# Performance work log

Hardware: AMD Instinct MI355X
Metric: run time of the kernel (lower is better)

Reference implementation:

```python
import jax, jax.numpy as jnp
import numpy as np

N, E = 50000, 800000
D_IN_N, D_IN_E, D_OUT = 64, 64, 64


def setup_inputs() -> dict:
    key = jax.random.key(0)
    ks = jax.random.split(key, 10)
    stdv = 1.0 / np.sqrt(D_OUT)
    u = lambda k, shape: jax.random.uniform(k, shape, jnp.float32, -stdv, stdv)
    return {
        "nf": jax.random.normal(ks[0], (N, D_IN_N), jnp.float32),
        "ef": jax.random.normal(ks[1], (E, D_IN_E), jnp.float32),
        "src": jax.random.randint(ks[2], (E,), 0, N, jnp.int32),
        "dst": jax.random.randint(ks[3], (E,), 0, N, jnp.int32),
        "W_node": u(ks[4], (D_IN_N, D_OUT)),
        "W_edge": u(ks[5], (D_IN_E, D_OUT)),
        "bias_node": u(ks[6], (D_OUT,)),
        "bias_edge": u(ks[7], (D_OUT,)),
        "W_dense": u(ks[8], (2 * D_OUT, D_OUT)),  # Linear(2*out, out) weight, stored transposed
        "b_dense": u(ks[9], (D_OUT,)),
    }


def reference(nf, ef, src, dst, W_node, W_edge, bias_node, bias_edge, W_dense, b_dense):
    n_nodes = nf.shape[0]
    # input projections
    nf_h = nf @ W_node                     # [N, D]
    ef_h = ef @ W_edge                     # [E, D]
    # update_all: mean of incoming edge features per dst node (0 for isolated nodes, DGL default)
    deg = jax.ops.segment_sum(jnp.ones((ef_h.shape[0],), ef_h.dtype), dst, num_segments=n_nodes)
    nb_ef = jax.ops.segment_sum(ef_h, dst, num_segments=n_nodes) / jnp.maximum(deg, 1.0)[:, None]
    # apply_nodes: nf = act(nf + bias)
    nf_out = jax.nn.relu(nf_h + bias_node)
    # apply_edges (uses updated nf): cat([ef + nb_ef[dst], (nf[src]+nf[dst])/2]) -> Linear -> +bias -> act
    tmp_ef = ef_h + nb_ef[dst]             # [E, D]
    srcdst_nf = (nf_out[src] + nf_out[dst]) * 0.5
    ef_out = jnp.concatenate([tmp_ef, srcdst_nf], axis=1) @ W_dense + b_dense + bias_edge
    ef_out = jax.nn.relu(ef_out)
    return nf_out, ef_out
```

## Files before the change

kernel.cpp:

```cpp
#include <hip/hip_runtime.h>

#define D 64

typedef __attribute__((ext_vector_type(8))) short short8;
typedef __attribute__((ext_vector_type(4))) float f32x4;

__device__ __forceinline__ ushort f2b(float f) {
    union { float f; unsigned u; } x; x.f = f;
    unsigned r = x.u + 0x7FFFu + ((x.u >> 16) & 1u);
    return (ushort)(r >> 16);
}
__device__ __forceinline__ float b2f(ushort u) {
    union { float f; unsigned u; } x; x.u = ((unsigned)u) << 16;
    return x.f;
}
__device__ __forceinline__ short8 pack8(float4 a, float4 b) {
    short8 r;
    r[0] = (short)f2b(a.x); r[1] = (short)f2b(a.y); r[2] = (short)f2b(a.z); r[3] = (short)f2b(a.w);
    r[4] = (short)f2b(b.x); r[5] = (short)f2b(b.y); r[6] = (short)f2b(b.z); r[7] = (short)f2b(b.w);
    return r;
}

__global__ __launch_bounds__(256) void setup_kernel(
    const float* __restrict__ W_edge, const float* __restrict__ W_dense,
    const float* __restrict__ b_dense, const float* __restrict__ bias_edge,
    ushort* __restrict__ Wcomb_b, float* __restrict__ bias2)
{
    const int tid = threadIdx.x;
    for (int idx = tid; idx < D * D; idx += 256) {
        int k = idx >> 6, n = idx & 63;
        float s = 0.f;
        #pragma unroll 8
        for (int j = 0; j < D; ++j)
            s = fmaf(W_edge[k * D + j], W_dense[j * D + n], s);
        Wcomb_b[n * D + k] = f2b(s);
    }
    if (tid < D) bias2[tid] = b_dense[tid] + bias_edge[tid];
}

__global__ __launch_bounds__(256) void node_proj_kernel(
    const float* __restrict__ nf, const float* __restrict__ Wn,
    const float* __restrict__ bias, const float* __restrict__ Wd_bot,
    float* __restrict__ out, ushort* __restrict__ nfp_b, int N)
{
    constexpr int ROWS = 16;
    __shared__ float Ws[D * D];
    __shared__ float Wb[D * D];
    __shared__ float As[ROWS * D];
    __shared__ float Vs[ROWS * D];
    const int tid = threadIdx.x;
    const long row0 = (long)blockIdx.x * ROWS;

    #pragma unroll
    for (int i = tid; i < D * D / 4; i += 256) {
        ((float4*)Ws)[i] = ((const float4*)Wn)[i];
        float4 v = ((const float4*)Wd_bot)[i];
        ((float4*)Wb)[i] = make_float4(0.5f * v.x, 0.5f * v.y, 0.5f * v.z, 0.5f * v.w);
    }
    {
        int i = tid;
        long r = row0 + (i * 4) / D;
        ((float4*)As)[i] = (r < N) ? ((const float4*)nf)[row0 * D / 4 + i]
                                   : make_float4(0.f, 0.f, 0.f, 0.f);
    }
    __syncthreads();

    const int c = tid & 63;
    const float b = bias[c];
    for (int rr = tid >> 6; rr < ROWS; rr += 4) {
        float acc = 0.f;
        #pragma unroll
        for (int k = 0; k < D; ++k)
            acc = fmaf(As[rr * D + k], Ws[k * D + c], acc);
        float v = fmaxf(acc + b, 0.f);
        Vs[rr * D + c] = v;
        long r = row0 + rr;
        if (r < N) out[r * D + c] = v;
    }
    __syncthreads();
    for (int rr = tid >> 6; rr < ROWS; rr += 4) {
        float acc = 0.f;
        #pragma unroll
        for (int k = 0; k < D; ++k)
            acc = fmaf(Vs[rr * D + k], Wb[k * D + c], acc);
        long r = row0 + rr;
        if (r < N) nfp_b[r * D + c] = f2b(acc);
    }
}

__global__ __launch_bounds__(256) void hist_kernel(
    const int* __restrict__ dst, int* __restrict__ deg_i, int E)
{
    int i = blockIdx.x * 256 + threadIdx.x;
    if (i < E) atomicAdd(deg_i + dst[i], 1);
}

__global__ __launch_bounds__(256) void scanA_kernel(
    const int* __restrict__ deg_i, int* __restrict__ pos,
    int* __restrict__ bsum, int N)
{
    __shared__ int s[256];
    const int tid = threadIdx.x;
    const int i = blockIdx.x * 256 + tid;
    int v = (i < N) ? deg_i[i] : 0;
    s[tid] = v;
    __syncthreads();
    #pragma unroll
    for (int off = 1; off < 256; off <<= 1) {
        int t = (tid >= off) ? s[tid - off] : 0;
        __syncthreads();
        s[tid] += t;
        __syncthreads();
    }
    if (i < N) pos[i] = s[tid] - v;
    if (tid == 255) bsum[blockIdx.x] = s[255];
}

__global__ __launch_bounds__(256) void scanB_kernel(int* __restrict__ bsum, int NB)
{
    __shared__ int s[256];
    const int tid = threadIdx.x;
    int v = (tid < NB) ? bsum[tid] : 0;
    s[tid] = v;
    __syncthreads();
    #pragma unroll
    for (int off = 1; off < 256; off <<= 1) {
        int t = (tid >= off) ? s[tid - off] : 0;
        __syncthreads();
        s[tid] += t;
        __syncthreads();
    }
    if (tid < NB) bsum[tid] = s[tid] - v;
}

__global__ __launch_bounds__(256) void scanC_kernel(
    const int* __restrict__ pos, int* __restrict__ cursor,
    const int* __restrict__ bsum, int N)
{
    int i = blockIdx.x * 256 + threadIdx.x;
    if (i < N) cursor[i] = pos[i] + bsum[blockIdx.x];
}

__global__ __launch_bounds__(256) void scatter_kernel(
    const int* __restrict__ dst, int* __restrict__ cursor,
    int2* __restrict__ sorted_ed, int E)
{
    int i = blockIdx.x * 256 + threadIdx.x;
    if (i < E) {
        int dv = dst[i];
        int slot = atomicAdd(cursor + dv, 1);
        sorted_ed[slot] = make_int2(i, dv);
    }
}

#define SEG_ROWS 128
__global__ __launch_bounds__(256) void efp_seg_kernel(
    const float* __restrict__ ef, const int2* __restrict__ sorted_ed,
    const ushort* __restrict__ Wt, ushort* __restrict__ efp,
    float* __restrict__ nb_sum, int E)
{
    __shared__ unsigned Slds[SEG_ROWS * 33];
    __shared__ int dsts[SEG_ROWS];
    const int tid = threadIdx.x;
    const long s0 = (long)blockIdx.x * SEG_ROWS;

    const int w = tid >> 6, lane = tid & 63;
    const int lr = lane & 15, g = lane >> 4;
    const bool odd = lane & 1;

    long gde[2];
    #pragma unroll
    for (int tt = 0; tt < 2; ++tt) {
        long s = s0 + 64 * tt + 16 * w + lr;
        if (s >= E) s = E - 1;
        gde[tt] = (long)sorted_ed[s].x;
    }
    float4 va[2][4];
    #pragma unroll
    for (int tt = 0; tt < 2; ++tt) {
        const float4* ap = (const float4*)(ef + gde[tt] * D);
        va[tt][0] = ap[2 * g];     va[tt][1] = ap[2 * g + 1];
        va[tt][2] = ap[8 + 2 * g]; va[tt][3] = ap[8 + 2 * g + 1];
    }
    int rbl[2]; long seo[2][2];
    #pragma unroll
    for (int tt = 0; tt < 2; ++tt) {
        rbl[tt] = 64 * tt + 16 * w + 4 * g + (odd ? 2 : 0);
        long s = s0 + rbl[tt];
        if (s > E - 2) s = (E - 2) & ~1L;
        int4 q = *(const int4*)&sorted_ed[s];
        seo[tt][0] = (long)q.x * D;
        seo[tt][1] = (long)q.z * D;
    }
    if (tid < SEG_ROWS) {
        long s = s0 + tid;
        dsts[tid] = (s < E) ? sorted_ed[s].y : -1;
    }

    short8 bf0[4], bf1[4];
    #pragma unroll
    for (int t = 0; t < 4; ++t) {
        bf0[t] = *(const short8*)&Wt[(16 * t + lr) * D + 8 * g];
        bf1[t] = *(const short8*)&Wt[(16 * t + lr) * D + 32 + 8 * g];
    }

    #pragma unroll
    for (int tt = 0; tt < 2; ++tt) {
        short8 a0 = pack8(va[tt][0], va[tt][1]);
        short8 a1 = pack8(va[tt][2], va[tt][3]);
        f32x4 acc[4];
        #pragma unroll
        for (int t = 0; t < 4; ++t) {
            f32x4 z = {0.f, 0.f, 0.f, 0.f};
            z = __builtin_amdgcn_mfma_f32_16x16x32_bf16(a0, bf0[t], z, 0, 0, 0);
            z = __builtin_amdgcn_mfma_f32_16x16x32_bf16(a1, bf1[t], z, 0, 0, 0);
            acc[t] = z;
        }

        const int rb = rbl[tt];
        long sl0 = s0 + rb, sl1 = s0 + rb + 1;
        #pragma unroll
        for (int t = 0; t < 4; ++t) {
            float p0 = __shfl_xor(acc[t][0], 1, 64);
            float p1 = __shfl_xor(acc[t][1], 1, 64);
            float p2 = __shfl_xor(acc[t][2], 1, 64);
            float p3 = __shfl_xor(acc[t][3], 1, 64);
            float lo0, hi0, lo1, hi1;
            if (odd) { lo0 = p2; hi0 = acc[t][2]; lo1 = p3; hi1 = acc[t][3]; }
            else     { lo0 = acc[t][0]; hi0 = p0; lo1 = acc[t][1]; hi1 = p1; }
            int cbase = 16 * t + (lr & ~1);
            int dc = cbase >> 1;
            unsigned dw0 = ((unsigned)f2b(hi0) << 16) | (unsigned)f2b(lo0);
            unsigned dw1 = ((unsigned)f2b(hi1) << 16) | (unsigned)f2b(lo1);
            if (sl0 < E) *(unsigned*)(efp + seo[tt][0] + cbase) = dw0;
            if (sl1 < E) *(unsigned*)(efp + seo[tt][1] + cbase) = dw1;
            Slds[rb * 33 + dc]       = dw0;
            Slds[(rb + 1) * 33 + dc] = dw1;
        }
    }
    __syncthreads();

    {
        const int dwc = tid & 31;
        const int r0 = (tid >> 5) * 16;
        float seg0 = 0.f, seg1 = 0.f;
        int cur = dsts[r0];
        #pragma unroll 4
        for (int r = r0; r < r0 + 16; ++r) {
            int dv = dsts[r];
            unsigned u = Slds[r * 33 + dwc];
            if (dv != cur) {
                if (cur >= 0) {
                    atomicAdd(nb_sum + (long)cur * D + 2 * dwc, seg0);
                    atomicAdd(nb_sum + (long)cur * D + 2 * dwc + 1, seg1);
                }
                seg0 = seg1 = 0.f;
                cur = dv;
            }
            seg0 += b2f((ushort)(u & 0xffff));
            seg1 += b2f((ushort)(u >> 16));
        }
        if (cur >= 0) {
            atomicAdd(nb_sum + (long)cur * D + 2 * dwc, seg0);
            atomicAdd(nb_sum + (long)cur * D + 2 * dwc + 1, seg1);
        }
    }
}

__global__ __launch_bounds__(256) void ndp_lite_kernel(
    const float* __restrict__ nb_sum, const int* __restrict__ deg_i,
    const ushort* __restrict__ nfp_b, ushort* __restrict__ ndp_b, int N)
{
    long i = (long)blockIdx.x * 256 + threadIdx.x;
    long node = i >> 3;
    int cb = (int)(i & 7);
    if (node >= N) return;
    float inv = 1.0f / fmaxf((float)deg_i[node], 1.0f);
    const float4* sp = (const float4*)(nb_sum + node * D + cb * 8);
    float4 x0 = sp[0], x1 = sp[1];
    short8 np = *(const short8*)(nfp_b + node * D + cb * 8);
    short8 r;
    r[0] = (short)f2b(x0.x * inv + b2f((ushort)np[0]));
    r[1] = (short)f2b(x0.y * inv + b2f((ushort)np[1]));
    r[2] = (short)f2b(x0.z * inv + b2f((ushort)np[2]));
    r[3] = (short)f2b(x0.w * inv + b2f((ushort)np[3]));
    r[4] = (short)f2b(x1.x * inv + b2f((ushort)np[4]));
    r[5] = (short)f2b(x1.y * inv + b2f((ushort)np[5]));
    r[6] = (short)f2b(x1.z * inv + b2f((ushort)np[6]));
    r[7] = (short)f2b(x1.w * inv + b2f((ushort)np[7]));
    *(short8*)(ndp_b + node * D + cb * 8) = r;
}

__global__ __launch_bounds__(256) void final_kernel(
    const ushort* __restrict__ efp, const int* __restrict__ src,
    const int* __restrict__ dst, const ushort* __restrict__ ndp_b,
    const ushort* __restrict__ nfp_b, const float* __restrict__ bias2,
    float* __restrict__ out, int E)
{
    long idx = (long)blockIdx.x * 256 + threadIdx.x;
    long e = idx >> 2;
    int q = (int)(idx & 3);
    if (e >= E) return;
    int dv = dst[e], sv = src[e];
    const short8* ep = (const short8*)(efp + e * D + q * 16);
    const short8* np = (const short8*)(ndp_b + (long)dv * D + q * 16);
    const short8* sp = (const short8*)(nfp_b + (long)sv * D + q * 16);
    short8 e0 = ep[0], e1 = ep[1];
    short8 n0 = np[0], n1 = np[1];
    short8 s0 = sp[0], s1 = sp[1];
    const float4* bp = (const float4*)(bias2 + q * 16);
    float4 b0 = bp[0], b1 = bp[1], b2 = bp[2], b3 = bp[3];

    float r[16];
    #pragma unroll
    for (int j = 0; j < 8; ++j) {
        r[j]     = b2f((ushort)e0[j]) + b2f((ushort)n0[j]) + b2f((ushort)s0[j]);
        r[8 + j] = b2f((ushort)e1[j]) + b2f((ushort)n1[j]) + b2f((ushort)s1[j]);
    }
    float4* op = (float4*)(out + e * D + q * 16);
    op[0] = make_float4(fmaxf(r[0] + b0.x, 0.f), fmaxf(r[1] + b0.y, 0.f),
                        fmaxf(r[2] + b0.z, 0.f), fmaxf(r[3] + b0.w, 0.f));
    op[1] = make_float4(fmaxf(r[4] + b1.x, 0.f), fmaxf(r[5] + b1.y, 0.f),
                        fmaxf(r[6] + b1.z, 0.f), fmaxf(r[7] + b1.w, 0.f));
    op[2] = make_float4(fmaxf(r[8] + b2.x, 0.f), fmaxf(r[9] + b2.y, 0.f),
                        fmaxf(r[10] + b2.z, 0.f), fmaxf(r[11] + b2.w, 0.f));
    op[3] = make_float4(fmaxf(r[12] + b3.x, 0.f), fmaxf(r[13] + b3.y, 0.f),
                        fmaxf(r[14] + b3.z, 0.f), fmaxf(r[15] + b3.w, 0.f));
}

extern "C" void kernel_launch(void* const* d_in, const int* in_sizes, int n_in,
                              void* d_out, int out_size, void* d_ws, size_t ws_size,
                              hipStream_t stream) {
    const float* nf        = (const float*)d_in[0];
    const float* ef        = (const float*)d_in[1];
    const int*   src       = (const int*)d_in[2];
    const int*   dst       = (const int*)d_in[3];
    const float* W_node    = (const float*)d_in[4];
    const float* W_edge    = (const float*)d_in[5];
    const float* bias_node = (const float*)d_in[6];
    const float* bias_edge = (const float*)d_in[7];
    const float* W_dense   = (const float*)d_in[8];
    const float* b_dense   = (const float*)d_in[9];

    const int N = in_sizes[0] / D;
    const int E = in_sizes[1] / D;
    const int NB = (N + 255) / 256;

    float* nf_out = (float*)d_out;
    float* ef_out = (float*)d_out + (size_t)N * D;

    char* p = (char*)d_ws;
    int*    deg_i    = (int*)p;     p += (size_t)N * 4;
    float*  nb_sum   = (float*)p;   p += (size_t)N * D * 4;
    size_t  zbytes   = (size_t)(p - (char*)d_ws);
    int*    pos      = (int*)p;     p += (size_t)N * 4;
    int*    cursor   = (int*)p;     p += (size_t)N * 4;
    int*    bsum     = (int*)p;     p += 256 * 4;
    int2*   sorted_ed= (int2*)p;    p += (size_t)E * 8;
    ushort* nfp_b    = (ushort*)p;  p += (size_t)N * D * 2;
    ushort* ndp_b    = (ushort*)p;  p += (size_t)N * D * 2;
    ushort* Wcomb_b  = (ushort*)p;  p += D * D * 2;
    float*  bias2    = (float*)p;   p += 256;
    ushort* efp      = (ushort*)p;

    hipMemsetAsync(d_ws, 0, zbytes, stream);

    setup_kernel<<<1, 256, 0, stream>>>(W_edge, W_dense, b_dense, bias_edge,
                                        Wcomb_b, bias2);
    node_proj_kernel<<<(N + 15) / 16, 256, 0, stream>>>(nf, W_node, bias_node,
                                                        W_dense + D * D, nf_out, nfp_b, N);
    hist_kernel<<<(E + 255) / 256, 256, 0, stream>>>(dst, deg_i, E);
    scanA_kernel<<<NB, 256, 0, stream>>>(deg_i, pos, bsum, N);
    scanB_kernel<<<1, 256, 0, stream>>>(bsum, NB);
    scanC_kernel<<<NB, 256, 0, stream>>>(pos, cursor, bsum, N);
    scatter_kernel<<<(E + 255) / 256, 256, 0, stream>>>(dst, cursor, sorted_ed, E);
    efp_seg_kernel<<<(E + SEG_ROWS - 1) / SEG_ROWS, 256, 0, stream>>>(
        ef, sorted_ed, Wcomb_b, efp, nb_sum, E);
    ndp_lite_kernel<<<(int)(((size_t)N * 8 + 255) / 256), 256, 0, stream>>>(
        nb_sum, deg_i, nfp_b, ndp_b, N);
    final_kernel<<<(int)(((size_t)E * 4 + 255) / 256), 256, 0, stream>>>(
        efp, src, dst, ndp_b, nfp_b, bias2, ef_out, E);
}
```

Measured before the change: 399.5 us.

## Fuse front kernels, split edge projection from segmented gather-reduce, add nontemporal stores

Merges the setup, node projection and degree histogram into one launch, using block-index ranges to pick the role of each block. The edge projection now streams ef in natural order and writes efp coalesced, replacing the fused kernel that gathered ef rows in dst-sorted order. A separate persistent kernel, capped at 1024 blocks, then gathers bf16 efp rows in sorted order with software prefetch and does the segmented atomic reduction into nb_sum. Output stores use nontemporal hints. This trades a gather of fp32 ef for a gather of half-size bf16 efp, at the cost of one extra pass over efp and one extra launch.

```diff
diff --git a/kernel.cpp b/kernel.cpp
--- a/kernel.cpp
+++ b/kernel.cpp
@@ -21,78 +21,75 @@
     return r;
 }
 
-__global__ __launch_bounds__(256) void setup_kernel(
-    const float* __restrict__ W_edge, const float* __restrict__ W_dense,
-    const float* __restrict__ b_dense, const float* __restrict__ bias_edge,
-    ushort* __restrict__ Wcomb_b, float* __restrict__ bias2)
-{
-    const int tid = threadIdx.x;
-    for (int idx = tid; idx < D * D; idx += 256) {
-        int k = idx >> 6, n = idx & 63;
-        float s = 0.f;
-        #pragma unroll 8
-        for (int j = 0; j < D; ++j)
-            s = fmaf(W_edge[k * D + j], W_dense[j * D + n], s);
-        Wcomb_b[n * D + k] = f2b(s);
-    }
-    if (tid < D) bias2[tid] = b_dense[tid] + bias_edge[tid];
-}
-
-__global__ __launch_bounds__(256) void node_proj_kernel(
+__global__ __launch_bounds__(256) void fused_front_kernel(
     const float* __restrict__ nf, const float* __restrict__ Wn,
-    const float* __restrict__ bias, const float* __restrict__ Wd_bot,
-    float* __restrict__ out, ushort* __restrict__ nfp_b, int N)
-{
-    constexpr int ROWS = 16;
+    const float* __restrict__ bias, const float* __restrict__ Wd,
+    float* __restrict__ out, ushort* __restrict__ nfp_b, int N,
+    const int* __restrict__ dst, int* __restrict__ deg_i, int E,
+    const float* __restrict__ W_edge, const float* __restrict__ b_dense,
+    const float* __restrict__ bias_edge, ushort* __restrict__ Wcomb_b,
+    float* __restrict__ bias2, int NPB, int HB)
+{
     __shared__ float Ws[D * D];
     __shared__ float Wb[D * D];
-    __shared__ float As[ROWS * D];
-    __shared__ float Vs[ROWS * D];
+    __shared__ float As[16 * D];
+    __shared__ float Vs[16 * D];
     const int tid = threadIdx.x;
-    const long row0 = (long)blockIdx.x * ROWS;
-
-    #pragma unroll
-    for (int i = tid; i < D * D / 4; i += 256) {
-        ((float4*)Ws)[i] = ((const float4*)Wn)[i];
-        float4 v = ((const float4*)Wd_bot)[i];
-        ((float4*)Wb)[i] = make_float4(0.5f * v.x, 0.5f * v.y, 0.5f * v.z, 0.5f * v.w);
-    }
-    {
-        int i = tid;
-        long r = row0 + (i * 4) / D;
-        ((float4*)As)[i] = (r < N) ? ((const float4*)nf)[row0 * D / 4 + i]
-                                   : make_float4(0.f, 0.f, 0.f, 0.f);
-    }
-    __syncthreads();
-
-    const int c = tid & 63;
-    const float b = bias[c];
-    for (int rr = tid >> 6; rr < ROWS; rr += 4) {
-        float acc = 0.f;
+    const int bid = blockIdx.x;
+
+    if (bid < NPB) {
+        constexpr int ROWS = 16;
+        const long row0 = (long)bid * ROWS;
+        const float* Wd_bot = Wd + D * D;
         #pragma unroll
-        for (int k = 0; k < D; ++k)
-            acc = fmaf(As[rr * D + k], Ws[k * D + c], acc);
-        float v = fmaxf(acc + b, 0.f);
-        Vs[rr * D + c] = v;
-        long r = row0 + rr;
-        if (r < N) out[r * D + c] = v;
-    }
-    __syncthreads();
-    for (int rr = tid >> 6; rr < ROWS; rr += 4) {
-        float acc = 0.f;
-        #pragma unroll
-        for (int k = 0; k < D; ++k)
-            acc = fmaf(Vs[rr * D + k], Wb[k * D + c], acc);
-        long r = row0 + rr;
-        if (r < N) nfp_b[r * D + c] = f2b(acc);
-    }
-}
-
-__global__ __launch_bounds__(256) void hist_kernel(
-    const int* __restrict__ dst, int* __restrict__ deg_i, int E)
-{
-    int i = blockIdx.x * 256 + threadIdx.x;
-    if (i < E) atomicAdd(deg_i + dst[i], 1);
+        for (int i = tid; i < D * D / 4; i += 256) {
+            ((float4*)Ws)[i] = ((const float4*)Wn)[i];
+            float4 v = ((const float4*)Wd_bot)[i];
+            ((float4*)Wb)[i] = make_float4(0.5f * v.x, 0.5f * v.y, 0.5f * v.z, 0.5f * v.w);
+        }
+        {
+            int i = tid;
+            long r = row0 + (i * 4) / D;
+            ((float4*)As)[i] = (r < N) ? ((const float4*)nf)[row0 * D / 4 + i]
+                                       : make_float4(0.f, 0.f, 0.f, 0.f);
+        }
+        __syncthreads();
+
+        const int c = tid & 63;
+        const float b = bias[c];
+        for (int rr = tid >> 6; rr < ROWS; rr += 4) {
+            float acc = 0.f;
+            #pragma unroll
+            for (int k = 0; k < D; ++k)
+                acc = fmaf(As[rr * D + k], Ws[k * D + c], acc);
+            float v = fmaxf(acc + b, 0.f);
+            Vs[rr * D + c] = v;
+            long r = row0 + rr;
+            if (r < N) __builtin_nontemporal_store(v, &out[r * D + c]);
+        }
+        __syncthreads();
+        for (int rr = tid >> 6; rr < ROWS; rr += 4) {
+            float acc = 0.f;
+            #pragma unroll
+            for (int k = 0; k < D; ++k)
+                acc = fmaf(Vs[rr * D + k], Wb[k * D + c], acc);
+            long r = row0 + rr;
+            if (r < N) nfp_b[r * D + c] = f2b(acc);
+        }
+    } else if (bid < NPB + HB) {
+        int i = (bid - NPB) * 256 + tid;
+        if (i < E) atomicAdd(deg_i + dst[i], 1);
+    } else {
+        for (int idx = tid; idx < D * D; idx += 256) {
+            int k = idx >> 6, n = idx & 63;
+            float s = 0.f;
+            #pragma unroll 8
+            for (int j = 0; j < D; ++j)
+                s = fmaf(W_edge[k * D + j], Wd[j * D + n], s);
+            Wcomb_b[n * D + k] = f2b(s);
+        }
+        if (tid < D) bias2[tid] = b_dense[tid] + bias_edge[tid];
+    }
 }
 
 __global__ __launch_bounds__(256) void scanA_kernel(
@@ -153,117 +150,135 @@
     }
 }
 
-#define SEG_ROWS 128
-__global__ __launch_bounds__(256) void efp_seg_kernel(
-    const float* __restrict__ ef, const int2* __restrict__ sorted_ed,
-    const ushort* __restrict__ Wt, ushort* __restrict__ efp,
-    float* __restrict__ nb_sum, int E)
-{
-    __shared__ unsigned Slds[SEG_ROWS * 33];
-    __shared__ int dsts[SEG_ROWS];
+__global__ __launch_bounds__(256) void efp_stream_kernel(
+    const float* __restrict__ ef, const ushort* __restrict__ Wt,
+    ushort* __restrict__ efp, int E)
+{
     const int tid = threadIdx.x;
-    const long s0 = (long)blockIdx.x * SEG_ROWS;
-
+    const long row0 = (long)blockIdx.x * 64;
     const int w = tid >> 6, lane = tid & 63;
     const int lr = lane & 15, g = lane >> 4;
+    const int arow = 16 * w + lr;
+    long era = row0 + arow; if (era >= E) era = E - 1;
+
+    const float4* ap = (const float4*)(ef + era * D);
+    float4 v0 = ap[2 * g], v1 = ap[2 * g + 1];
+    float4 v2 = ap[8 + 2 * g], v3 = ap[8 + 2 * g + 1];
+    short8 a0 = pack8(v0, v1), a1 = pack8(v2, v3);
+
+    f32x4 acc[4];
+    #pragma unroll
+    for (int t = 0; t < 4; ++t) {
+        f32x4 z = {0.f, 0.f, 0.f, 0.f};
+        short8 b0 = *(const short8*)&Wt[(16 * t + lr) * D + 8 * g];
+        short8 b1 = *(const short8*)&Wt[(16 * t + lr) * D + 32 + 8 * g];
+        z = __builtin_amdgcn_mfma_f32_16x16x32_bf16(a0, b0, z, 0, 0, 0);
+        z = __builtin_amdgcn_mfma_f32_16x16x32_bf16(a1, b1, z, 0, 0, 0);
+        acc[t] = z;
+    }
+
     const bool odd = lane & 1;
-
-    long gde[2];
-    #pragma unroll
-    for (int tt = 0; tt < 2; ++tt) {
-        long s = s0 + 64 * tt + 16 * w + lr;
+    const int rb = 16 * w + 4 * g + (odd ? 2 : 0);
+    long e0 = row0 + rb, e1 = row0 + rb + 1;
+    #pragma unroll
+    for (int t = 0; t < 4; ++t) {
+        float p0 = __shfl_xor(acc[t][0], 1, 64);
+        float p1 = __shfl_xor(acc[t][1], 1, 64);
+        float p2 = __shfl_xor(acc[t][2], 1, 64);
+        float p3 = __shfl_xor(acc[t][3], 1, 64);
+        float lo0, hi0, lo1, hi1;
+        if (odd) { lo0 = p2; hi0 = acc[t][2]; lo1 = p3; hi1 = acc[t][3]; }
+        else     { lo0 = acc[t][0]; hi0 = p0; lo1 = acc[t][1]; hi1 = p1; }
+        int cbase = 16 * t + (lr & ~1);
+        unsigned dw0 = ((unsigned)f2b(hi0) << 16) | (unsigned)f2b(lo0);
+        unsigned dw1 = ((unsigned)f2b(hi1) << 16) | (unsigned)f2b(lo1);
+        if (e0 < E) *(unsigned*)(efp + e0 * D + cbase) = dw0;
+        if (e1 < E) *(unsigned*)(efp + e1 * D + cbase) = dw1;
+    }
+}
+
+#define SG_CH 128
+__global__ __launch_bounds__(256) void seg_gather_kernel(
+    const ushort* __restrict__ efp, const int2* __restrict__ sorted_ed,
+    float* __restrict__ nb_sum, int E, int nch, int stride)
+{
+    __shared__ unsigned Slds[SG_CH * 36];
+    __shared__ int dsts[SG_CH];
+    const int tid = threadIdx.x;
+    const int r_ = tid >> 3, c8 = tid & 7;
+
+    int c = blockIdx.x;
+    if (c >= nch) return;
+
+    int2 id[4]; short8 row[4];
+    #pragma unroll
+    for (int p = 0; p < 4; ++p) {
+        long s = (long)c * SG_CH + r_ + 32 * p;
         if (s >= E) s = E - 1;
-        gde[tt] = (long)sorted_ed[s].x;
-    }
-    float4 va[2][4];
-    #pragma unroll
-    for (int tt = 0; tt < 2; ++tt) {
-        const float4* ap = (const float4*)(ef + gde[tt] * D);
-        va[tt][0] = ap[2 * g];     va[tt][1] = ap[2 * g + 1];
-        va[tt][2] = ap[8 + 2 * g]; va[tt][3] = ap[8 + 2 * g + 1];
-    }
-    int rbl[2]; long seo[2][2];
-    #pragma unroll
-    for (int tt = 0; tt < 2; ++tt) {
-        rbl[tt] = 64 * tt + 16 * w + 4 * g + (odd ? 2 : 0);
-        long s = s0 + rbl[tt];
-        if (s > E - 2) s = (E - 2) & ~1L;
-        int4 q = *(const int4*)&sorted_ed[s];
-        seo[tt][0] = (long)q.x * D;
-        seo[tt][1] = (long)q.z * D;
-    }
-    if (tid < SEG_ROWS) {
-        long s = s0 + tid;
-        dsts[tid] = (s < E) ? sorted_ed[s].y : -1;
-    }
-
-    short8 bf0[4], bf1[4];
-    #pragma unroll
-    for (int t = 0; t < 4; ++t) {
-        bf0[t] = *(const short8*)&Wt[(16 * t + lr) * D + 8 * g];
-        bf1[t] = *(const short8*)&Wt[(16 * t + lr) * D + 32 + 8 * g];
-    }
-
-    #pragma unroll
-    for (int tt = 0; tt < 2; ++tt) {
-        short8 a0 = pack8(va[tt][0], va[tt][1]);
-        short8 a1 = pack8(va[tt][2], va[tt][3]);
-        f32x4 acc[4];
+        id[p] = sorted_ed[s];
+    }
+    #pragma unroll
+    for (int p = 0; p < 4; ++p)
+        row[p] = *(const short8*)(efp + (long)id[p].x * D + c8 * 8);
+
+    while (true) {
+        const int cn = c + stride;
+        const bool more = (cn < nch);
+        int2 idn[4];
+        if (more) {
+            #pragma unroll
+            for (int p = 0; p < 4; ++p) {
+                long s = (long)cn * SG_CH + r_ + 32 * p;
+                if (s >= E) s = E - 1;
+                idn[p] = sorted_ed[s];
+            }
+        }
         #pragma unroll
-        for (int t = 0; t < 4; ++t) {
-            f32x4 z = {0.f, 0.f, 0.f, 0.f};
-            z = __builtin_amdgcn_mfma_f32_16x16x32_bf16(a0, bf0[t], z, 0, 0, 0);
-            z = __builtin_amdgcn_mfma_f32_16x16x32_bf16(a1, bf1[t], z, 0, 0, 0);
-            acc[t] = z;
-        }
-
-        const int rb = rbl[tt];
-        long sl0 = s0 + rb, sl1 = s0 + rb + 1;
+        for (int p = 0; p < 4; ++p) {
+            int r = r_ + 32 * p;
+            *(uint4*)&Slds[r * 36 + c8 * 4] = *(uint4*)&row[p];
+            if (c8 == 0) {
+                long s = (long)c * SG_CH + r;
+                dsts[r] = (s < E) ? id[p].y : -1;
+            }
+        }
+        __syncthreads();
+        short8 rown[4];
+        if (more) {
+            #pragma unroll
+            for (int p = 0; p < 4; ++p)
+                rown[p] = *(const short8*)(efp + (long)idn[p].x * D + c8 * 8);
+        }
+        {
+            const int dwc = tid & 31;
+            const int r0 = (tid >> 5) * 16;
+            float seg0 = 0.f, seg1 = 0.f;
+            int cur = dsts[r0];
+            #pragma unroll 4
+            for (int r = r0; r < r0 + 16; ++r) {
+                int dv = dsts[r];
+                unsigned u = Slds[r * 36 + dwc];
+                if (dv != cur) {
+                    if (cur >= 0) {
+                        atomicAdd(nb_sum + (long)cur * D + 2 * dwc, seg0);
+                        atomicAdd(nb_sum + (long)cur * D + 2 * dwc + 1, seg1);
+                    }
+                    seg0 = seg1 = 0.f;
+                    cur = dv;
+                }
+                seg0 += b2f((ushort)(u & 0xffff));
+                seg1 += b2f((ushort)(u >> 16));
+            }
+            if (cur >= 0) {
+                atomicAdd(nb_sum + (long)cur * D + 2 * dwc, seg0);
+                atomicAdd(nb_sum + (long)cur * D + 2 * dwc + 1, seg1);
+            }
+        }
+        __syncthreads();
+        if (!more) break;
+        c = cn;
         #pragma unroll
-        for (int t = 0; t < 4; ++t) {
-            float p0 = __shfl_xor(acc[t][0], 1, 64);
-            float p1 = __shfl_xor(acc[t][1], 1, 64);
-            float p2 = __shfl_xor(acc[t][2], 1, 64);
-            float p3 = __shfl_xor(acc[t][3], 1, 64);
-            float lo0, hi0, lo1, hi1;
-            if (odd) { lo0 = p2; hi0 = acc[t][2]; lo1 = p3; hi1 = acc[t][3]; }
-            else     { lo0 = acc[t][0]; hi0 = p0; lo1 = acc[t][1]; hi1 = p1; }
-            int cbase = 16 * t + (lr & ~1);
-            int dc = cbase >> 1;
-            unsigned dw0 = ((unsigned)f2b(hi0) << 16) | (unsigned)f2b(lo0);
-            unsigned dw1 = ((unsigned)f2b(hi1) << 16) | (unsigned)f2b(lo1);
-            if (sl0 < E) *(unsigned*)(efp + seo[tt][0] + cbase) = dw0;
-            if (sl1 < E) *(unsigned*)(efp + seo[tt][1] + cbase) = dw1;
-            Slds[rb * 33 + dc]       = dw0;
-            Slds[(rb + 1) * 33 + dc] = dw1;
-        }
-    }
-    __syncthreads();
-
-    {
-        const int dwc = tid & 31;
-        const int r0 = (tid >> 5) * 16;
-        float seg0 = 0.f, seg1 = 0.f;
-        int cur = dsts[r0];
-        #pragma unroll 4
-        for (int r = r0; r < r0 + 16; ++r) {
-            int dv = dsts[r];
-            unsigned u = Slds[r * 33 + dwc];
-            if (dv != cur) {
-                if (cur >= 0) {
-                    atomicAdd(nb_sum + (long)cur * D + 2 * dwc, seg0);
-                    atomicAdd(nb_sum + (long)cur * D + 2 * dwc + 1, seg1);
-                }
-                seg0 = seg1 = 0.f;
-                cur = dv;
-            }
-            seg0 += b2f((ushort)(u & 0xffff));
-            seg1 += b2f((ushort)(u >> 16));
-        }
-        if (cur >= 0) {
-            atomicAdd(nb_sum + (long)cur * D + 2 * dwc, seg0);
-            atomicAdd(nb_sum + (long)cur * D + 2 * dwc + 1, seg1);
-        }
+        for (int p = 0; p < 4; ++p) { id[p] = idn[p]; row[p] = rown[p]; }
     }
 }
 
@@ -317,15 +332,19 @@
         r[j]     = b2f((ushort)e0[j]) + b2f((ushort)n0[j]) + b2f((ushort)s0[j]);
         r[8 + j] = b2f((ushort)e1[j]) + b2f((ushort)n1[j]) + b2f((ushort)s1[j]);
     }
-    float4* op = (float4*)(out + e * D + q * 16);
-    op[0] = make_float4(fmaxf(r[0] + b0.x, 0.f), fmaxf(r[1] + b0.y, 0.f),
-                        fmaxf(r[2] + b0.z, 0.f), fmaxf(r[3] + b0.w, 0.f));
-    op[1] = make_float4(fmaxf(r[4] + b1.x, 0.f), fmaxf(r[5] + b1.y, 0.f),
-                        fmaxf(r[6] + b1.z, 0.f), fmaxf(r[7] + b1.w, 0.f));
-    op[2] = make_float4(fmaxf(r[8] + b2.x, 0.f), fmaxf(r[9] + b2.y, 0.f),
-                        fmaxf(r[10] + b2.z, 0.f), fmaxf(r[11] + b2.w, 0.f));
-    op[3] = make_float4(fmaxf(r[12] + b3.x, 0.f), fmaxf(r[13] + b3.y, 0.f),
-                        fmaxf(r[14] + b3.z, 0.f), fmaxf(r[15] + b3.w, 0.f));
+    f32x4* op = (f32x4*)(out + e * D + q * 16);
+    f32x4 o0 = {fmaxf(r[0] + b0.x, 0.f), fmaxf(r[1] + b0.y, 0.f),
+                fmaxf(r[2] + b0.z, 0.f), fmaxf(r[3] + b0.w, 0.f)};
+    f32x4 o1 = {fmaxf(r[4] + b1.x, 0.f), fmaxf(r[5] + b1.y, 0.f),
+                fmaxf(r[6] + b1.z, 0.f), fmaxf(r[7] + b1.w, 0.f)};
+    f32x4 o2 = {fmaxf(r[8] + b2.x, 0.f), fmaxf(r[9] + b2.y, 0.f),
+                fmaxf(r[10] + b2.z, 0.f), fmaxf(r[11] + b2.w, 0.f)};
+    f32x4 o3 = {fmaxf(r[12] + b3.x, 0.f), fmaxf(r[13] + b3.y, 0.f),
+                fmaxf(r[14] + b3.z, 0.f), fmaxf(r[15] + b3.w, 0.f)};
+    __builtin_nontemporal_store(o0, op + 0);
+    __builtin_nontemporal_store(o1, op + 1);
+    __builtin_nontemporal_store(o2, op + 2);
+    __builtin_nontemporal_store(o3, op + 3);
 }
 
 extern "C" void kernel_launch(void* const* d_in, const int* in_sizes, int n_in,
@@ -345,6 +364,8 @@
     const int N = in_sizes[0] / D;
     const int E = in_sizes[1] / D;
     const int NB = (N + 255) / 256;
+    const int NPB = (N + 15) / 16;
+    const int HB = (E + 255) / 256;
 
     float* nf_out = (float*)d_out;
     float* ef_out = (float*)d_out + (size_t)N * D;
@@ -365,17 +386,19 @@
 
     hipMemsetAsync(d_ws, 0, zbytes, stream);
 
-    setup_kernel<<<1, 256, 0, stream>>>(W_edge, W_dense, b_dense, bias_edge,
-                                        Wcomb_b, bias2);
-    node_proj_kernel<<<(N + 15) / 16, 256, 0, stream>>>(nf, W_node, bias_node,
-                                                        W_dense + D * D, nf_out, nfp_b, N);
-    hist_kernel<<<(E + 255) / 256, 256, 0, stream>>>(dst, deg_i, E);
+    fused_front_kernel<<<NPB + HB + 1, 256, 0, stream>>>(
+        nf, W_node, bias_node, W_dense, nf_out, nfp_b, N,
+        dst, deg_i, E, W_edge, b_dense, bias_edge, Wcomb_b, bias2, NPB, HB);
     scanA_kernel<<<NB, 256, 0, stream>>>(deg_i, pos, bsum, N);
     scanB_kernel<<<1, 256, 0, stream>>>(bsum, NB);
     scanC_kernel<<<NB, 256, 0, stream>>>(pos, cursor, bsum, N);
     scatter_kernel<<<(E + 255) / 256, 256, 0, stream>>>(dst, cursor, sorted_ed, E);
-    efp_seg_kernel<<<(E + SEG_ROWS - 1) / SEG_ROWS, 256, 0, stream>>>(
-        ef, sorted_ed, Wcomb_b, efp, nb_sum, E);
+    efp_stream_kernel<<<(E + 63) / 64, 256, 0, stream>>>(ef, Wcomb_b, efp, E);
+    {
+        const int nch = (E + SG_CH - 1) / SG_CH;
+        const int grid = nch < 1024 ? nch : 1024;
+        seg_gather_kernel<<<grid, 256, 0, stream>>>(efp, sorted_ed, nb_sum, E, nch, grid);
+    }
     ndp_lite_kernel<<<(int)(((size_t)N * 8 + 255) / 256), 256, 0, stream>>>(
         nb_sum, deg_i, nfp_b, ndp_b, N);
     final_kernel<<<(int)(((size_t)E * 4 + 255) / 256), 256, 0, stream>>>(
```

Measured after the change: 463.6 us. 16.0% more time.
